# Optimization experiments

Measured on AMD Instinct MI355X. Metric: run time of the kernel, lower is better.

The kernel has to match this reference:

```python
import jax, jax.numpy as jnp
import numpy as np

BATCH = 8
IN_FEATURES = 4096
OUT_FEATURES = 16384


def setup_inputs() -> dict:
    key = jax.random.key(0)
    k1, k2, k3 = jax.random.split(key, 3)
    # activations, fp16 (w4a16 path)
    x = jax.random.normal(k1, (BATCH, IN_FEATURES), dtype=jnp.float16)
    # packed int4 weights: each element holds two signed 4-bit values
    # (low nibble = even column 2k, high nibble = odd column 2k+1)
    weight = jax.random.randint(k2, (OUT_FEATURES, IN_FEATURES // 2), 0, 256, dtype=jnp.int32)
    # per-output-channel symmetric scales (small positive values)
    weight_scales = (jax.random.uniform(k3, (OUT_FEATURES,), dtype=jnp.float16) * jnp.float16(0.01)
                     + jnp.float16(0.001))
    return {"x": x, "weight": weight, "weight_scales": weight_scales}


def _dequant_i4(weight, scales):
    """Unpack two signed int4 per byte and apply per-row scales.
    weight: [out, in//2] int32 (byte values 0..255); scales: [out] fp16.
    Returns [out, in] in scales.dtype.
    """
    low = weight & 0xF
    high = (weight >> 4) & 0xF
    # sign-extend 4-bit two's complement (the torch module stores signed int4;
    # mask 0x88 XOR in the kernel is the equivalent sign-bit flip)
    low = jnp.where(low >= 8, low - 16, low)
    high = jnp.where(high >= 8, high - 16, high)
    w = jnp.stack([low, high], axis=-1).reshape(weight.shape[0], -1)  # [out, in]
    return w.astype(scales.dtype) * scales[:, None]


def reference(x, weight, weight_scales):
    W = _dequant_i4(weight, weight_scales)           # [out, in] fp16
    return jnp.matmul(x, W.T)                         # [batch, out] fp16
```

## Files before the change

### kernel.cpp

```cpp
#include <hip/hip_runtime.h>
#include <hip/hip_bf16.h>
#include <stdint.h>

#define BATCH 8
#define K_DIM 4096
#define N_DIM 16384
#define KH (K_DIM / 2)
#define BLOCK 512
#define ROWS_PER_WAVE 4
#define ROWS_PER_BLOCK 32
#define ITERS (KH / 4 / 64)

__device__ __forceinline__ float bf16lo(uint32_t u) { return __uint_as_float(u << 16); }
__device__ __forceinline__ float bf16hi(uint32_t u) { return __uint_as_float(u & 0xFFFF0000u); }

__device__ __forceinline__ uint32_t f32_to_bf16_bits(float f) {
    uint32_t u = __float_as_uint(f);
    return (u + 0x7FFFu + ((u >> 16) & 1u)) >> 16;
}

__global__ __launch_bounds__(BLOCK, 2)
void w4a16_gemv(const float* __restrict__ x,
                const int*   __restrict__ w,
                const float* __restrict__ scales,
                float*       __restrict__ out)
{
    __shared__ uint4 xchunks[K_DIM];
    const int tid = threadIdx.x;

    #pragma unroll
    for (int t = 0; t < K_DIM / BLOCK; ++t) {
        const int c = t * BLOCK + tid;
        float v[BATCH];
        #pragma unroll
        for (int b = 0; b < BATCH; ++b) v[b] = x[b * K_DIM + c];
        uint4 pk;
        pk.x = f32_to_bf16_bits(v[0]) | (f32_to_bf16_bits(v[1]) << 16);
        pk.y = f32_to_bf16_bits(v[2]) | (f32_to_bf16_bits(v[3]) << 16);
        pk.z = f32_to_bf16_bits(v[4]) | (f32_to_bf16_bits(v[5]) << 16);
        pk.w = f32_to_bf16_bits(v[6]) | (f32_to_bf16_bits(v[7]) << 16);
        xchunks[c ^ ((c >> 3) & 7)] = pk;
    }
    __syncthreads();

    const int wave = tid >> 6;
    const int lane = tid & 63;
    const int row0 = blockIdx.x * ROWS_PER_BLOCK + wave * ROWS_PER_WAVE;

    const int4* __restrict__ wv0 = (const int4*)(w + (size_t)(row0 + 0) * KH);
    const int4* __restrict__ wv1 = (const int4*)(w + (size_t)(row0 + 1) * KH);
    const int4* __restrict__ wv2 = (const int4*)(w + (size_t)(row0 + 2) * KH);
    const int4* __restrict__ wv3 = (const int4*)(w + (size_t)(row0 + 3) * KH);

    float acc[ROWS_PER_WAVE][BATCH];
    #pragma unroll
    for (int j = 0; j < ROWS_PER_WAVE; ++j)
        #pragma unroll
        for (int b = 0; b < BATCH; ++b) acc[j][b] = 0.0f;

    #pragma unroll 1
    for (int t = 0; t < ITERS; ++t) {
        const int u = (t << 6) + lane;
        int4 q0 = wv0[u];
        int4 q1 = wv1[u];
        int4 q2 = wv2[u];
        int4 q3 = wv3[u];
        const int xork  = u & 7;
        const int cbase = u << 3;

        int qw[ROWS_PER_WAVE][4];
        qw[0][0] = q0.x; qw[0][1] = q0.y; qw[0][2] = q0.z; qw[0][3] = q0.w;
        qw[1][0] = q1.x; qw[1][1] = q1.y; qw[1][2] = q1.z; qw[1][3] = q1.w;
        qw[2][0] = q2.x; qw[2][1] = q2.y; qw[2][2] = q2.z; qw[2][3] = q2.w;
        qw[3][0] = q3.x; qw[3][1] = q3.y; qw[3][2] = q3.z; qw[3][3] = q3.w;

        #pragma unroll
        for (int m = 0; m < 4; ++m) {
            const uint4 xa = xchunks[cbase + ((2 * m)     ^ xork)];
            const uint4 xb = xchunks[cbase + ((2 * m + 1) ^ xork)];

            float xlo[BATCH], xhi[BATCH];
            xlo[0] = bf16lo(xa.x); xlo[1] = bf16hi(xa.x);
            xlo[2] = bf16lo(xa.y); xlo[3] = bf16hi(xa.y);
            xlo[4] = bf16lo(xa.z); xlo[5] = bf16hi(xa.z);
            xlo[6] = bf16lo(xa.w); xlo[7] = bf16hi(xa.w);
            xhi[0] = bf16lo(xb.x); xhi[1] = bf16hi(xb.x);
            xhi[2] = bf16lo(xb.y); xhi[3] = bf16hi(xb.y);
            xhi[4] = bf16lo(xb.z); xhi[5] = bf16hi(xb.z);
            xhi[6] = bf16lo(xb.w); xhi[7] = bf16hi(xb.w);

            #pragma unroll
            for (int j = 0; j < ROWS_PER_WAVE; ++j) {
                const unsigned bv = ((unsigned)qw[j][m]) & 0xFFu;
                const float flo = (float)((int)((bv & 0xFu) ^ 8u) - 8);
                const float fhi = (float)((int)(((bv >> 4) & 0xFu) ^ 8u) - 8);
                #pragma unroll
                for (int b = 0; b < BATCH; ++b) {
                    acc[j][b] = fmaf(flo, xlo[b], acc[j][b]);
                    acc[j][b] = fmaf(fhi, xhi[b], acc[j][b]);
                }
            }
        }
    }

    float vals[32];
    #pragma unroll
    for (int j = 0; j < ROWS_PER_WAVE; ++j)
        #pragma unroll
        for (int b = 0; b < BATCH; ++b) vals[j * 8 + b] = acc[j][b];

    #pragma unroll
    for (int k = 0; k < 5; ++k) {
        const int sel = (lane >> k) & 1;
        const int n = 32 >> k;
        #pragma unroll
        for (int i = 0; i < n / 2; ++i) {
            const float a = vals[2 * i];
            const float c = vals[2 * i + 1];
            const float mine  = sel ? c : a;
            const float other = sel ? a : c;
            vals[i] = mine + __shfl_xor(other, 1 << k, 64);
        }
    }
    const float total = vals[0] + __shfl_xor(vals[0], 32, 64);

    if (lane < 32) {
        const int r = row0 + (lane >> 3);
        out[(size_t)(lane & 7) * N_DIM + r] = total * scales[r];
    }
}

extern "C" void kernel_launch(void* const* d_in, const int* in_sizes, int n_in,
                              void* d_out, int out_size, void* d_ws, size_t ws_size,
                              hipStream_t stream) {
    const float* x      = (const float*)d_in[0];
    const int*   w      = (const int*)d_in[1];
    const float* scales = (const float*)d_in[2];
    float*       out    = (float*)d_out;

    dim3 grid(N_DIM / ROWS_PER_BLOCK);
    dim3 block(BLOCK);
    hipLaunchKernelGGL(w4a16_gemv, grid, block, 0, stream, x, w, scales, out);
}
```

Measured before the change: 197.5 us.

## Double-buffer weight loads and use packed float2 FMAs in the GEMV loop

Software-pipelines the int4 weight loads with two register buffers, so the next iteration's global loads are issued before the current one's compute. The FMA inner loop now uses two-wide float vectors, meant to map to packed FMA instructions. Sign extension of the nibbles switches to shift-based arithmetic, and the LDS swizzle key is hoisted out of the loop. Holding a second buffer raises VGPR use, which may cut occupancy under the 2-block launch bound.

```diff
diff --git a/kernel.cpp b/kernel.cpp
--- a/kernel.cpp
+++ b/kernel.cpp
@@ -10,6 +10,8 @@
 #define ROWS_PER_WAVE 4
 #define ROWS_PER_BLOCK 32
 #define ITERS (KH / 4 / 64)
+
+typedef __attribute__((ext_vector_type(2))) float f32x2;
 
 __device__ __forceinline__ float bf16lo(uint32_t u) { return __uint_as_float(u << 16); }
 __device__ __forceinline__ float bf16hi(uint32_t u) { return __uint_as_float(u & 0xFFFF0000u); }
@@ -46,68 +48,81 @@
     const int wave = tid >> 6;
     const int lane = tid & 63;
     const int row0 = blockIdx.x * ROWS_PER_BLOCK + wave * ROWS_PER_WAVE;
+    const int xork = lane & 7;
 
     const int4* __restrict__ wv0 = (const int4*)(w + (size_t)(row0 + 0) * KH);
     const int4* __restrict__ wv1 = (const int4*)(w + (size_t)(row0 + 1) * KH);
     const int4* __restrict__ wv2 = (const int4*)(w + (size_t)(row0 + 2) * KH);
     const int4* __restrict__ wv3 = (const int4*)(w + (size_t)(row0 + 3) * KH);
 
-    float acc[ROWS_PER_WAVE][BATCH];
+    f32x2 acc2[ROWS_PER_WAVE][BATCH / 2];
     #pragma unroll
     for (int j = 0; j < ROWS_PER_WAVE; ++j)
         #pragma unroll
-        for (int b = 0; b < BATCH; ++b) acc[j][b] = 0.0f;
+        for (int p = 0; p < BATCH / 2; ++p) acc2[j][p] = (f32x2){0.0f, 0.0f};
 
-    #pragma unroll 1
-    for (int t = 0; t < ITERS; ++t) {
-        const int u = (t << 6) + lane;
-        int4 q0 = wv0[u];
-        int4 q1 = wv1[u];
-        int4 q2 = wv2[u];
-        int4 q3 = wv3[u];
-        const int xork  = u & 7;
+    auto compute = [&](const int4 (&q)[ROWS_PER_WAVE], int t) {
+        const int u     = (t << 6) + lane;
         const int cbase = u << 3;
-
         int qw[ROWS_PER_WAVE][4];
-        qw[0][0] = q0.x; qw[0][1] = q0.y; qw[0][2] = q0.z; qw[0][3] = q0.w;
-        qw[1][0] = q1.x; qw[1][1] = q1.y; qw[1][2] = q1.z; qw[1][3] = q1.w;
-        qw[2][0] = q2.x; qw[2][1] = q2.y; qw[2][2] = q2.z; qw[2][3] = q2.w;
-        qw[3][0] = q3.x; qw[3][1] = q3.y; qw[3][2] = q3.z; qw[3][3] = q3.w;
-
+        #pragma unroll
+        for (int j = 0; j < ROWS_PER_WAVE; ++j) {
+            qw[j][0] = q[j].x; qw[j][1] = q[j].y; qw[j][2] = q[j].z; qw[j][3] = q[j].w;
+        }
         #pragma unroll
         for (int m = 0; m < 4; ++m) {
             const uint4 xa = xchunks[cbase + ((2 * m)     ^ xork)];
             const uint4 xb = xchunks[cbase + ((2 * m + 1) ^ xork)];
-
-            float xlo[BATCH], xhi[BATCH];
-            xlo[0] = bf16lo(xa.x); xlo[1] = bf16hi(xa.x);
-            xlo[2] = bf16lo(xa.y); xlo[3] = bf16hi(xa.y);
-            xlo[4] = bf16lo(xa.z); xlo[5] = bf16hi(xa.z);
-            xlo[6] = bf16lo(xa.w); xlo[7] = bf16hi(xa.w);
-            xhi[0] = bf16lo(xb.x); xhi[1] = bf16hi(xb.x);
-            xhi[2] = bf16lo(xb.y); xhi[3] = bf16hi(xb.y);
-            xhi[4] = bf16lo(xb.z); xhi[5] = bf16hi(xb.z);
-            xhi[6] = bf16lo(xb.w); xhi[7] = bf16hi(xb.w);
-
+            f32x2 xlo2[4], xhi2[4];
+            xlo2[0] = (f32x2){bf16lo(xa.x), bf16hi(xa.x)};
+            xlo2[1] = (f32x2){bf16lo(xa.y), bf16hi(xa.y)};
+            xlo2[2] = (f32x2){bf16lo(xa.z), bf16hi(xa.z)};
+            xlo2[3] = (f32x2){bf16lo(xa.w), bf16hi(xa.w)};
+            xhi2[0] = (f32x2){bf16lo(xb.x), bf16hi(xb.x)};
+            xhi2[1] = (f32x2){bf16lo(xb.y), bf16hi(xb.y)};
+            xhi2[2] = (f32x2){bf16lo(xb.z), bf16hi(xb.z)};
+            xhi2[3] = (f32x2){bf16lo(xb.w), bf16hi(xb.w)};
             #pragma unroll
             for (int j = 0; j < ROWS_PER_WAVE; ++j) {
-                const unsigned bv = ((unsigned)qw[j][m]) & 0xFFu;
-                const float flo = (float)((int)((bv & 0xFu) ^ 8u) - 8);
-                const float fhi = (float)((int)(((bv >> 4) & 0xFu) ^ 8u) - 8);
+                const uint32_t bv = ((uint32_t)qw[j][m]) & 0xFFu;
+                const float flo = (float)((int)(bv << 28) >> 28);
+                const float fhi = (float)((int)(bv << 24) >> 28);
+                const f32x2 flo2 = (f32x2){flo, flo};
+                const f32x2 fhi2 = (f32x2){fhi, fhi};
                 #pragma unroll
-                for (int b = 0; b < BATCH; ++b) {
-                    acc[j][b] = fmaf(flo, xlo[b], acc[j][b]);
-                    acc[j][b] = fmaf(fhi, xhi[b], acc[j][b]);
+                for (int p = 0; p < BATCH / 2; ++p) {
+                    acc2[j][p] = __builtin_elementwise_fma(flo2, xlo2[p], acc2[j][p]);
+                    acc2[j][p] = __builtin_elementwise_fma(fhi2, xhi2[p], acc2[j][p]);
                 }
             }
         }
+    };
+
+    int4 qa[ROWS_PER_WAVE], qb[ROWS_PER_WAVE];
+    qa[0] = wv0[lane]; qa[1] = wv1[lane]; qa[2] = wv2[lane]; qa[3] = wv3[lane];
+
+    #pragma unroll 1
+    for (int t = 0; t < ITERS; t += 2) {
+        {
+            const int un = ((t + 1) << 6) + lane;
+            qb[0] = wv0[un]; qb[1] = wv1[un]; qb[2] = wv2[un]; qb[3] = wv3[un];
+        }
+        compute(qa, t);
+        if (t + 2 < ITERS) {
+            const int un = ((t + 2) << 6) + lane;
+            qa[0] = wv0[un]; qa[1] = wv1[un]; qa[2] = wv2[un]; qa[3] = wv3[un];
+        }
+        compute(qb, t + 1);
     }
 
     float vals[32];
     #pragma unroll
     for (int j = 0; j < ROWS_PER_WAVE; ++j)
         #pragma unroll
-        for (int b = 0; b < BATCH; ++b) vals[j * 8 + b] = acc[j][b];
+        for (int p = 0; p < BATCH / 2; ++p) {
+            vals[j * 8 + 2 * p]     = acc2[j][p].x;
+            vals[j * 8 + 2 * p + 1] = acc2[j][p].y;
+        }
 
     #pragma unroll
     for (int k = 0; k < 5; ++k) {
```

After: 198.8 us. Within noise of the previous version (+0.7%).
